# Kernel tuning notes

Hardware: AMD Instinct MI355X
Metric: run time of the kernel (lower is better)

Reference implementation:

```python
import jax, jax.numpy as jnp
import numpy as np

N = 16384
N_ITER = 10
TAU = 1e-3  # LM initial damping factor


def _skew(w):
    z = jnp.zeros((), w.dtype)
    return jnp.stack([
        jnp.stack([z, -w[2], w[1]]),
        jnp.stack([w[2], z, -w[0]]),
        jnp.stack([-w[1], w[0], z]),
    ])


def se3_exp(x):
    # x = [omega (3), v (3)] -> 4x4 SE3 (lie_se3_to_SE3)
    w, v = x[:3], x[3:]
    th2 = jnp.dot(w, w)
    th = jnp.sqrt(th2)
    small = th < 1e-8
    ths = jnp.where(small, jnp.ones_like(th), th)
    A = jnp.where(small, 1.0 - th2 / 6.0, jnp.sin(ths) / ths)
    B = jnp.where(small, 0.5 - th2 / 24.0, (1.0 - jnp.cos(ths)) / ths ** 2)
    C = jnp.where(small, 1.0 / 6.0 - th2 / 120.0, (ths - jnp.sin(ths)) / ths ** 3)
    W = _skew(w)
    W2 = W @ W
    I = jnp.eye(3, dtype=x.dtype)
    R = I + A * W + B * W2
    V = I + B * W + C * W2
    t = V @ v
    T = jnp.eye(4, dtype=x.dtype).at[:3, :3].set(R).at[:3, 3].set(t)
    return T


def _res_jac(x, ref_pts, trg_pts, trg_normals):
    T = se3_exp(x)
    R, t = T[:3, :3], T[:3, 3]
    # dist_association: ref cloud transformed by inv(T_est), nearest target point
    Ri, ti = R.T, -R.T @ t
    ref_t = ref_pts @ Ri.T + ti  # [N,3]
    d2 = ((ref_t ** 2).sum(-1)[:, None]
          + (trg_pts ** 2).sum(-1)[None, :]
          - 2.0 * (ref_t @ trg_pts.T))  # [N_ref, N_trg] -- dominant memory traffic
    trg_ids = jnp.argmin(d2, axis=1)  # src_ids == arange(N_ref)
    # residual: dot(n_trg_transformed, ref - trg_transformed) at correspondences
    trg_t = trg_pts @ R.T + t
    n_t = trg_normals @ R.T
    n = n_t[trg_ids]          # [N,3] gather
    p = trg_t[trg_ids]        # [N,3] gather
    r = jnp.sum(n * (ref_pts - p), axis=1)  # [N]
    # J = n^T @ j_3d(ref_pts)  ==  [cross(p_ref, n), n]  (closed form of 1x3x6 matmuls)
    J = jnp.concatenate([jnp.cross(ref_pts, n), n], axis=1)  # [N,6]
    return r, J


def reference(ref_pts, trg_pts, trg_normals):
    dtype = ref_pts.dtype
    x = jnp.zeros(6, dtype=dtype)
    r, J = _res_jac(x, ref_pts, trg_pts, trg_normals)
    F = jnp.sum(r ** 2)
    H0 = J.T @ J
    mu = TAU * jnp.max(jnp.diag(H0))
    nu = jnp.asarray(2.0, dtype)
    I6 = jnp.eye(6, dtype=dtype)
    for _ in range(N_ITER):
        H = J.T @ J
        g = J.T @ r
        dx = jnp.linalg.solve(H + mu * I6, -g)
        x_new = x + dx
        r_new, J_new = _res_jac(x_new, ref_pts, trg_pts, trg_normals)
        F_new = jnp.sum(r_new ** 2)
        denom = jnp.dot(dx, mu * dx - g)
        rho = (F - F_new) / jnp.where(jnp.abs(denom) < 1e-12, 1e-12, denom)
        accept = rho > 0.0
        x = jnp.where(accept, x_new, x)
        r = jnp.where(accept, r_new, r)
        J = jnp.where(accept, J_new, J)
        F = jnp.where(accept, F_new, F)
        mu = jnp.where(accept,
                       mu * jnp.maximum(1.0 / 3.0, 1.0 - (2.0 * rho - 1.0) ** 3),
                       mu * nu)
        nu = jnp.where(accept, jnp.asarray(2.0, dtype), 2.0 * nu)
    T = se3_exp(x)
    cost = jnp.mean(r ** 2)  # cost_fun(residual_fun(x,...))
    return T, cost


def setup_inputs() -> dict:
    key = jax.random.key(0)
    k1, k2 = jax.random.split(key)
    ref_pts = jax.random.normal(k1, (N, 3), dtype=jnp.float32)
    # target = slightly rotated/translated copy so ICP has a meaningful solution
    ang = 0.05
    R_true = np.array([[np.cos(ang), -np.sin(ang), 0.0],
                       [np.sin(ang), np.cos(ang), 0.0],
                       [0.0, 0.0, 1.0]], dtype=np.float32)
    t_true = np.array([0.02, -0.01, 0.03], dtype=np.float32)
    trg_pts = ref_pts @ jnp.asarray(R_true).T + jnp.asarray(t_true)
    n = jax.random.normal(k2, (N, 3), dtype=jnp.float32)
    trg_normals = n / jnp.linalg.norm(n, axis=1, keepdims=True)
    return {"ref_pts": ref_pts, "trg_pts": trg_pts, "trg_normals": trg_normals}
```

## Files before the change

### kernel.cpp

```cpp
#include <hip/hip_runtime.h>
#include <stdint.h>

#define N_PTS 16384
#define TAU_C 0.001f
#define N_ITER 10

#define G 48
#define NCELLS (G * G * G)
#define XMIN (-6.0f)
#define CELL_H 0.25f
#define INV_H 4.0f
#define NSCAN ((NCELLS + 1023) / 1024)
#define GS 8
#define QPB (256 / GS)
#define NEVAL (N_PTS / QPB)

struct State {
  float x[6];
  float xc[6];
  float dx[6];
  float Rc[9];
  float tc[3];
  float H[21];
  float g[6];
  float F, mu, nu;
};

__device__ void se3_exp_rt(const float* x, float* R, float* t) {
  float wx = x[0], wy = x[1], wz = x[2];
  float vx = x[3], vy = x[4], vz = x[5];
  float th2 = wx*wx + wy*wy + wz*wz;
  float th = sqrtf(th2);
  float A, B, C;
  if (th < 1e-8f) {
    A = 1.0f - th2 / 6.0f;
    B = 0.5f - th2 / 24.0f;
    C = 1.0f / 6.0f - th2 / 120.0f;
  } else {
    float s = sinf(th), c = cosf(th);
    A = s / th;
    B = (1.0f - c) / th2;
    C = (th - s) / (th2 * th);
  }
  float W[9]  = {0.f, -wz, wy,  wz, 0.f, -wx,  -wy, wx, 0.f};
  float W2[9];
  #pragma unroll
  for (int r = 0; r < 3; r++)
    #pragma unroll
    for (int c = 0; c < 3; c++)
      W2[3*r+c] = W[3*r+0]*W[0+c] + W[3*r+1]*W[3+c] + W[3*r+2]*W[6+c];
  float V[9];
  #pragma unroll
  for (int k = 0; k < 9; k++) {
    float I = (k == 0 || k == 4 || k == 8) ? 1.f : 0.f;
    R[k] = I + A * W[k] + B * W2[k];
    V[k] = I + B * W[k] + C * W2[k];
  }
  t[0] = V[0]*vx + V[1]*vy + V[2]*vz;
  t[1] = V[3]*vx + V[4]*vy + V[5]*vz;
  t[2] = V[6]*vx + V[7]*vy + V[8]*vz;
}

__device__ inline int cell1d(float v) {
  int c = (int)floorf((v - XMIN) * INV_H);
  return min(max(c, 0), G - 1);
}

__global__ __launch_bounds__(256) void zero_kernel(unsigned* __restrict__ count,
                                                   unsigned* __restrict__ counter,
                                                   State* st) {
  unsigned idx = blockIdx.x * 256u + threadIdx.x;
  if (idx < NCELLS) count[idx] = 0u;
  if (idx == 0) {
    #pragma unroll
    for (int k = 0; k < 6; k++) { st->x[k] = 0.f; st->xc[k] = 0.f; st->dx[k] = 0.f; }
    #pragma unroll
    for (int k = 0; k < 9; k++) st->Rc[k] = (k % 4 == 0) ? 1.f : 0.f;
    st->tc[0] = st->tc[1] = st->tc[2] = 0.f;
    st->nu = 2.f;
    *counter = 0u;
  }
}

__global__ __launch_bounds__(256) void count_kernel(const float* __restrict__ trg,
                                                    unsigned* __restrict__ count) {
  int j = blockIdx.x * 256 + threadIdx.x;
  int cx = cell1d(trg[3*j]), cy = cell1d(trg[3*j+1]), cz = cell1d(trg[3*j+2]);
  atomicAdd(&count[(cz * G + cy) * G + cx], 1u);
}

__global__ __launch_bounds__(256) void scan1_kernel(const unsigned* __restrict__ count,
                                                    unsigned* __restrict__ excl,
                                                    unsigned* __restrict__ blockSums) {
  __shared__ unsigned sh[256];
  const int t = threadIdx.x;
  const unsigned base = blockIdx.x * 1024u + t * 4u;
  unsigned v0 = (base + 0 < NCELLS) ? count[base + 0] : 0u;
  unsigned v1 = (base + 1 < NCELLS) ? count[base + 1] : 0u;
  unsigned v2 = (base + 2 < NCELLS) ? count[base + 2] : 0u;
  unsigned v3 = (base + 3 < NCELLS) ? count[base + 3] : 0u;
  unsigned tsum = v0 + v1 + v2 + v3;
  sh[t] = tsum;
  __syncthreads();
  for (int off = 1; off < 256; off <<= 1) {
    unsigned xv = (t >= off) ? sh[t - off] : 0u;
    __syncthreads();
    sh[t] += xv;
    __syncthreads();
  }
  unsigned texcl = sh[t] - tsum;
  if (t == 255) blockSums[blockIdx.x] = sh[255];
  if (base + 0 < NCELLS) excl[base + 0] = texcl;
  if (base + 1 < NCELLS) excl[base + 1] = texcl + v0;
  if (base + 2 < NCELLS) excl[base + 2] = texcl + v0 + v1;
  if (base + 3 < NCELLS) excl[base + 3] = texcl + v0 + v1 + v2;
}

__global__ __launch_bounds__(512) void scan2_kernel(unsigned* __restrict__ blockSums) {
  __shared__ unsigned sh[512];
  int t = threadIdx.x;
  unsigned v = (t < NSCAN) ? blockSums[t] : 0u;
  sh[t] = v;
  __syncthreads();
  for (int off = 1; off < 512; off <<= 1) {
    unsigned xv = (t >= off) ? sh[t - off] : 0u;
    __syncthreads();
    sh[t] += xv;
    __syncthreads();
  }
  if (t < NSCAN) blockSums[t] = sh[t] - v;
}

__global__ __launch_bounds__(256) void scan3_kernel(const unsigned* __restrict__ count,
                                                    unsigned* __restrict__ cursor,
                                                    const unsigned* __restrict__ blockSums,
                                                    unsigned* __restrict__ gridPacked) {
  const unsigned base = blockIdx.x * 1024u + threadIdx.x * 4u;
  unsigned boff = blockSums[blockIdx.x];
  #pragma unroll
  for (int q = 0; q < 4; q++) {
    unsigned idx = base + q;
    if (idx < NCELLS) {
      unsigned start = cursor[idx] + boff;
      unsigned n = count[idx]; n = n > 255u ? 255u : n;
      gridPacked[idx] = (start << 8) | n;
      cursor[idx] = start;
    }
  }
}

__global__ __launch_bounds__(256) void scatter_kernel(const float* __restrict__ trg,
                                                      unsigned* __restrict__ cursor,
                                                      float4* __restrict__ sortedPts,
                                                      unsigned* __restrict__ sortedIdx) {
  int j = blockIdx.x * 256 + threadIdx.x;
  float tx = trg[3*j], ty = trg[3*j+1], tz = trg[3*j+2];
  int cx = cell1d(tx), cy = cell1d(ty), cz = cell1d(tz);
  unsigned pos = atomicAdd(&cursor[(cz * G + cy) * G + cx], 1u);
  sortedPts[pos] = make_float4(tx, ty, tz, __uint_as_float((unsigned)j));
  sortedIdx[pos] = (unsigned)j;
}

__global__ __launch_bounds__(256) void eval_kernel(const float* __restrict__ ref,
                                                   const float* __restrict__ trg,
                                                   const float* __restrict__ nrm,
                                                   const unsigned* __restrict__ gridPacked,
                                                   const float4* __restrict__ sortedPts,
                                                   const unsigned* __restrict__ sortedIdx,
                                                   State* st,
                                                   double* __restrict__ partials,
                                                   unsigned* __restrict__ counter,
                                                   float* out, int mode) {
  const int tid = threadIdx.x;
  const int gl = tid & (GS - 1);
  const int it = blockIdx.x * QPB + (tid >> 3);
  const int i = (int)sortedIdx[it];

  const float R00 = st->Rc[0], R01 = st->Rc[1], R02 = st->Rc[2];
  const float R10 = st->Rc[3], R11 = st->Rc[4], R12 = st->Rc[5];
  const float R20 = st->Rc[6], R21 = st->Rc[7], R22 = st->Rc[8];
  const float t0 = st->tc[0], t1 = st->tc[1], t2 = st->tc[2];

  const float rx = ref[3*i], ry = ref[3*i+1], rz = ref[3*i+2];
  const float ax = rx - t0, ay = ry - t1, az = rz - t2;
  const float qx = R00*ax + R10*ay + R20*az;
  const float qy = R01*ax + R11*ay + R21*az;
  const float qz = R02*ax + R12*ay + R22*az;
  const int gx = cell1d(qx), gy = cell1d(qy), gz = cell1d(qz);

  unsigned long long bkey = 0xFFFFFFFFFFFFFFFFULL;
  for (int r = 1; r <= G; r++) {
    const int W = 2*r + 1, W2 = W * W, nc = W2 * W;
    for (int t = gl; t < nc; t += GS) {
      int tz = t / W2;
      int rm = t - tz * W2;
      int ty = rm / W;
      int tx = rm - ty * W;
      int cz = gz + tz - r, cy = gy + ty - r, cx = gx + tx - r;
      if ((unsigned)cx >= (unsigned)G || (unsigned)cy >= (unsigned)G ||
          (unsigned)cz >= (unsigned)G) continue;
      unsigned pc = gridPacked[(cz * G + cy) * G + cx];
      unsigned s0 = pc >> 8, n = pc & 255u;
      for (unsigned c = 0; c < n; c++) {
        float4 p = sortedPts[s0 + c];
        float ddx = qx - p.x, ddy = qy - p.y, ddz = qz - p.z;
        float d2 = fmaf(ddz, ddz, fmaf(ddy, ddy, ddx * ddx));
        unsigned long long key = ((unsigned long long)__float_as_uint(d2) << 32)
                               | (unsigned long long)__float_as_uint(p.w);
        bkey = key < bkey ? key : bkey;
      }
    }
    #pragma unroll
    for (int off = 1; off < GS; off <<= 1) {
      unsigned long long o = __shfl_xor(bkey, off, 64);
      bkey = o < bkey ? o : bkey;
    }
    float best = __uint_as_float((unsigned)(bkey >> 32));
    float dmin = 3.4e38f;
    if (gx - r > 0)     dmin = fminf(dmin, qx - (XMIN + (float)(gx - r) * CELL_H));
    if (gx + r < G - 1) dmin = fminf(dmin, (XMIN + (float)(gx + r + 1) * CELL_H) - qx);
    if (gy - r > 0)     dmin = fminf(dmin, qy - (XMIN + (float)(gy - r) * CELL_H));
    if (gy + r < G - 1) dmin = fminf(dmin, (XMIN + (float)(gy + r + 1) * CELL_H) - qy);
    if (gz - r > 0)     dmin = fminf(dmin, qz - (XMIN + (float)(gz - r) * CELL_H));
    if (gz + r < G - 1) dmin = fminf(dmin, (XMIN + (float)(gz + r + 1) * CELL_H) - qz);
    if (best <= dmin * dmin) break;
  }
  const int j = (int)(unsigned)(bkey & 0xFFFFFFFFULL);

  float Jv[6] = {0.f, 0.f, 0.f, 0.f, 0.f, 0.f};
  float rres = 0.f;
  if (gl == 0) {
    float nx0 = nrm[3*j], ny0 = nrm[3*j+1], nz0 = nrm[3*j+2];
    float sx = trg[3*j], sy = trg[3*j+1], sz = trg[3*j+2];
    float nx = R00*nx0 + R01*ny0 + R02*nz0;
    float ny = R10*nx0 + R11*ny0 + R12*nz0;
    float nz = R20*nx0 + R21*ny0 + R22*nz0;
    float pxx = R00*sx + R01*sy + R02*sz + t0;
    float pyy = R10*sx + R11*sy + R12*sz + t1;
    float pzz = R20*sx + R21*sy + R22*sz + t2;
    float dxx = rx - pxx, dyy = ry - pyy, dzz = rz - pzz;
    rres = nx*dxx + ny*dyy + nz*dzz;
    Jv[0] = ry*nz - rz*ny;
    Jv[1] = rz*nx - rx*nz;
    Jv[2] = rx*ny - ry*nx;
    Jv[3] = nx; Jv[4] = ny; Jv[5] = nz;
  }

  double acc[28];
  int c21 = 0;
  #pragma unroll
  for (int a = 0; a < 6; a++)
    #pragma unroll
    for (int b = a; b < 6; b++)
      acc[c21++] = (double)Jv[a] * (double)Jv[b];
  #pragma unroll
  for (int a = 0; a < 6; a++) acc[21+a] = (double)Jv[a] * (double)rres;
  acc[27] = (double)rres * (double)rres;

  #pragma unroll
  for (int kk = 0; kk < 28; kk++) {
    double v = acc[kk];
    for (int off = 32; off; off >>= 1) v += __shfl_down(v, off);
    acc[kk] = v;
  }
  __shared__ double redD[4][28];
  int wave = tid >> 6, lane = tid & 63;
  if (lane == 0) {
    #pragma unroll
    for (int kk = 0; kk < 28; kk++) redD[wave][kk] = acc[kk];
  }
  __syncthreads();
  if (tid < 28)
    partials[tid * NEVAL + blockIdx.x] =
        redD[0][tid] + redD[1][tid] + redD[2][tid] + redD[3][tid];

  __shared__ bool last;
  __syncthreads();
  if (tid == 0) {
    __threadfence();
    unsigned old = atomicAdd(counter, 1u);
    last = (old == NEVAL - 1);
  }
  __syncthreads();
  if (!last) return;

  __threadfence();
  __shared__ double red2[28][8];
  if (tid < 224) {
    int c = tid >> 3, s = tid & 7;
    double sum = 0.0;
    const double* pp = partials + c * NEVAL + s * 64;
    for (int b = 0; b < 64; b++) sum += pp[b];
    red2[c][s] = sum;
  }
  __syncthreads();
  __shared__ float tot[28];
  if (tid < 28) {
    double s = 0.0;
    #pragma unroll
    for (int k = 0; k < 8; k++) s += red2[tid][k];
    tot[tid] = (float)s;
  }
  __syncthreads();

  if (tid == 0) {
    atomicExch(counter, 0u);
    float Fn = tot[27];
    float mu, nu;

    if (mode == 0) {
      #pragma unroll
      for (int k = 0; k < 6; k++) st->x[k] = st->xc[k];
      #pragma unroll
      for (int k = 0; k < 21; k++) st->H[k] = tot[k];
      #pragma unroll
      for (int k = 0; k < 6; k++) st->g[k] = tot[21+k];
      st->F = Fn;
      float md = tot[0];
      md = fmaxf(md, tot[6]); md = fmaxf(md, tot[11]); md = fmaxf(md, tot[15]);
      md = fmaxf(md, tot[18]); md = fmaxf(md, tot[20]);
      mu = TAU_C * md;
      nu = 2.f;
    } else {
      mu = st->mu; nu = st->nu;
      float denom = 0.f;
      #pragma unroll
      for (int k = 0; k < 6; k++) denom += st->dx[k] * (mu * st->dx[k] - st->g[k]);
      if (fabsf(denom) < 1e-12f) denom = 1e-12f;
      float rho = (st->F - Fn) / denom;
      if (rho > 0.f) {
        #pragma unroll
        for (int k = 0; k < 6; k++) st->x[k] = st->xc[k];
        #pragma unroll
        for (int k = 0; k < 21; k++) st->H[k] = tot[k];
        #pragma unroll
        for (int k = 0; k < 6; k++) st->g[k] = tot[21+k];
        st->F = Fn;
        float tcube = 2.f * rho - 1.f;
        mu = mu * fmaxf(1.f / 3.f, 1.f - tcube * tcube * tcube);
        nu = 2.f;
      } else {
        mu = mu * nu;
        nu = 2.f * nu;
      }
    }
    st->mu = mu; st->nu = nu;

    if (mode < N_ITER) {
      float A[6][7];
      int c21b = 0;
      #pragma unroll
      for (int a = 0; a < 6; a++)
        #pragma unroll
        for (int b = a; b < 6; b++) { A[a][b] = st->H[c21b]; A[b][a] = st->H[c21b]; c21b++; }
      #pragma unroll
      for (int a = 0; a < 6; a++) { A[a][a] += mu; A[a][6] = -st->g[a]; }
      #pragma unroll
      for (int col = 0; col < 6; col++) {
        float inv = 1.f / A[col][col];
        #pragma unroll
        for (int rI = 0; rI < 6; rI++) {
          if (rI > col) {
            float f = A[rI][col] * inv;
            #pragma unroll
            for (int cc = 0; cc < 7; cc++)
              if (cc >= col) A[rI][cc] -= f * A[col][cc];
          }
        }
      }
      float d[6];
      #pragma unroll
      for (int rI = 5; rI >= 0; rI--) {
        float s = A[rI][6];
        #pragma unroll
        for (int cc = 0; cc < 6; cc++)
          if (cc > rI) s -= A[rI][cc] * d[cc];
        d[rI] = s / A[rI][rI];
      }
      float Rn[9], tn[3];
      #pragma unroll
      for (int k = 0; k < 6; k++) { st->dx[k] = d[k]; st->xc[k] = st->x[k] + d[k]; }
      se3_exp_rt(st->xc, Rn, tn);
      #pragma unroll
      for (int k = 0; k < 9; k++) st->Rc[k] = Rn[k];
      #pragma unroll
      for (int k = 0; k < 3; k++) st->tc[k] = tn[k];
    } else {
      float Rn[9], tn[3];
      se3_exp_rt(st->x, Rn, tn);
      out[0] = Rn[0]; out[1] = Rn[1]; out[2]  = Rn[2]; out[3]  = tn[0];
      out[4] = Rn[3]; out[5] = Rn[4]; out[6]  = Rn[5]; out[7]  = tn[1];
      out[8] = Rn[6]; out[9] = Rn[7]; out[10] = Rn[8]; out[11] = tn[2];
      out[12] = 0.f; out[13] = 0.f; out[14] = 0.f; out[15] = 1.f;
      out[16] = st->F / (float)N_PTS;
    }
  }
}

extern "C" void kernel_launch(void* const* d_in, const int* in_sizes, int n_in,
                              void* d_out, int out_size, void* d_ws, size_t ws_size,
                              hipStream_t stream) {
  const float* ref = (const float*)d_in[0];
  const float* trg = (const float*)d_in[1];
  const float* nrm = (const float*)d_in[2];
  float* out = (float*)d_out;

  char* ws = (char*)d_ws;
  unsigned* count      = (unsigned*)(ws);
  unsigned* gridPacked = (unsigned*)(ws + 442368);
  unsigned* cursor     = (unsigned*)(ws + 884736);
  unsigned* blockSums  = (unsigned*)(ws + 1327104);
  float4*   sortedPts  = (float4*)  (ws + 1329152);
  unsigned* sortedIdx  = (unsigned*)(ws + 1591296);
  double*   partials   = (double*)  (ws + 1656832);
  unsigned* counter    = (unsigned*)(ws + 1771520);
  State*    st         = (State*)   (ws + 1771584);

  zero_kernel   <<<(NCELLS + 255) / 256, 256, 0, stream>>>(count, counter, st);
  count_kernel  <<<N_PTS / 256, 256, 0, stream>>>(trg, count);
  scan1_kernel  <<<NSCAN, 256, 0, stream>>>(count, cursor, blockSums);
  scan2_kernel  <<<1, 512, 0, stream>>>(blockSums);
  scan3_kernel  <<<NSCAN, 256, 0, stream>>>(count, cursor, blockSums, gridPacked);
  scatter_kernel<<<N_PTS / 256, 256, 0, stream>>>(trg, cursor, sortedPts, sortedIdx);

  for (int e = 0; e <= N_ITER; e++)
    eval_kernel<<<NEVAL, 256, 0, stream>>>(ref, trg, nrm, gridPacked, sortedPts,
                                           sortedIdx, st, partials, counter, out, e);
}
```

Before: 394.7 us.

## Search fixed 3x3x3 neighborhood with 16 lanes, brute-force fallback for unresolved queries

Result: slower. 721.6 us (+82.8%).

```diff
diff --git a/kernel.cpp b/kernel.cpp
--- a/kernel.cpp
+++ b/kernel.cpp
@@ -11,7 +11,7 @@
 #define CELL_H 0.25f
 #define INV_H 4.0f
 #define NSCAN ((NCELLS + 1023) / 1024)
-#define GS 8
+#define GS 16
 #define QPB (256 / GS)
 #define NEVAL (N_PTS / QPB)
 
@@ -172,8 +172,9 @@
                                                    unsigned* __restrict__ counter,
                                                    float* out, int mode) {
   const int tid = threadIdx.x;
+  const int lane = tid & 63;
   const int gl = tid & (GS - 1);
-  const int it = blockIdx.x * QPB + (tid >> 3);
+  const int it = blockIdx.x * QPB + (tid >> 4);
   const int i = (int)sortedIdx[it];
 
   const float R00 = st->Rc[0], R01 = st->Rc[1], R02 = st->Rc[2];
@@ -188,42 +189,70 @@
   const float qz = R02*ax + R12*ay + R22*az;
   const int gx = cell1d(qx), gy = cell1d(qy), gz = cell1d(qz);
 
+  unsigned pcv[2];
+  #pragma unroll
+  for (int k = 0; k < 2; k++) {
+    pcv[k] = 0u;
+    int t = gl + GS * k;
+    if (t < 27) {
+      int tz = t / 9, rm = t - tz * 9, ty = rm / 3, tx = rm - ty * 3;
+      int cz = gz + tz - 1, cy = gy + ty - 1, cx = gx + tx - 1;
+      if ((unsigned)cx < (unsigned)G && (unsigned)cy < (unsigned)G &&
+          (unsigned)cz < (unsigned)G)
+        pcv[k] = gridPacked[(cz * G + cy) * G + cx];
+    }
+  }
   unsigned long long bkey = 0xFFFFFFFFFFFFFFFFULL;
-  for (int r = 1; r <= G; r++) {
-    const int W = 2*r + 1, W2 = W * W, nc = W2 * W;
-    for (int t = gl; t < nc; t += GS) {
-      int tz = t / W2;
-      int rm = t - tz * W2;
-      int ty = rm / W;
-      int tx = rm - ty * W;
-      int cz = gz + tz - r, cy = gy + ty - r, cx = gx + tx - r;
-      if ((unsigned)cx >= (unsigned)G || (unsigned)cy >= (unsigned)G ||
-          (unsigned)cz >= (unsigned)G) continue;
-      unsigned pc = gridPacked[(cz * G + cy) * G + cx];
-      unsigned s0 = pc >> 8, n = pc & 255u;
-      for (unsigned c = 0; c < n; c++) {
-        float4 p = sortedPts[s0 + c];
-        float ddx = qx - p.x, ddy = qy - p.y, ddz = qz - p.z;
-        float d2 = fmaf(ddz, ddz, fmaf(ddy, ddy, ddx * ddx));
-        unsigned long long key = ((unsigned long long)__float_as_uint(d2) << 32)
-                               | (unsigned long long)__float_as_uint(p.w);
-        bkey = key < bkey ? key : bkey;
-      }
-    }
-    #pragma unroll
-    for (int off = 1; off < GS; off <<= 1) {
-      unsigned long long o = __shfl_xor(bkey, off, 64);
-      bkey = o < bkey ? o : bkey;
-    }
-    float best = __uint_as_float((unsigned)(bkey >> 32));
-    float dmin = 3.4e38f;
-    if (gx - r > 0)     dmin = fminf(dmin, qx - (XMIN + (float)(gx - r) * CELL_H));
-    if (gx + r < G - 1) dmin = fminf(dmin, (XMIN + (float)(gx + r + 1) * CELL_H) - qx);
-    if (gy - r > 0)     dmin = fminf(dmin, qy - (XMIN + (float)(gy - r) * CELL_H));
-    if (gy + r < G - 1) dmin = fminf(dmin, (XMIN + (float)(gy + r + 1) * CELL_H) - qy);
-    if (gz - r > 0)     dmin = fminf(dmin, qz - (XMIN + (float)(gz - r) * CELL_H));
-    if (gz + r < G - 1) dmin = fminf(dmin, (XMIN + (float)(gz + r + 1) * CELL_H) - qz);
-    if (best <= dmin * dmin) break;
+  #pragma unroll
+  for (int k = 0; k < 2; k++) {
+    unsigned s0 = pcv[k] >> 8, n = pcv[k] & 255u;
+    for (unsigned c = 0; c < n; c++) {
+      float4 p = sortedPts[s0 + c];
+      float ddx = qx - p.x, ddy = qy - p.y, ddz = qz - p.z;
+      float d2 = fmaf(ddz, ddz, fmaf(ddy, ddy, ddx * ddx));
+      unsigned long long key = ((unsigned long long)__float_as_uint(d2) << 32)
+                             | (unsigned long long)(unsigned)__float_as_uint(p.w);
+      bkey = key < bkey ? key : bkey;
+    }
+  }
+  #pragma unroll
+  for (int off = 1; off < GS; off <<= 1) {
+    unsigned long long o = __shfl_xor(bkey, off, 64);
+    bkey = o < bkey ? o : bkey;
+  }
+  float best = __uint_as_float((unsigned)(bkey >> 32));
+  float dmin = 3.4e38f;
+  if (gx - 1 > 0)     dmin = fminf(dmin, qx - (XMIN + (float)(gx - 1) * CELL_H));
+  if (gx + 1 < G - 1) dmin = fminf(dmin, (XMIN + (float)(gx + 2) * CELL_H) - qx);
+  if (gy - 1 > 0)     dmin = fminf(dmin, qy - (XMIN + (float)(gy - 1) * CELL_H));
+  if (gy + 1 < G - 1) dmin = fminf(dmin, (XMIN + (float)(gy + 2) * CELL_H) - qy);
+  if (gz - 1 > 0)     dmin = fminf(dmin, qz - (XMIN + (float)(gz - 1) * CELL_H));
+  if (gz + 1 < G - 1) dmin = fminf(dmin, (XMIN + (float)(gz + 2) * CELL_H) - qz);
+  bool resolved = (best <= dmin * dmin);
+
+  unsigned long long m = __ballot((gl == 0) && !resolved);
+  while (m) {
+    int src = __ffsll((long long)m) - 1;
+    m &= m - 1;
+    float bqx = __shfl(qx, src, 64);
+    float bqy = __shfl(qy, src, 64);
+    float bqz = __shfl(qz, src, 64);
+    unsigned long long bb = 0xFFFFFFFFFFFFFFFFULL;
+    #pragma unroll 4
+    for (int p = lane; p < N_PTS; p += 64) {
+      float4 pt = sortedPts[p];
+      float ddx = bqx - pt.x, ddy = bqy - pt.y, ddz = bqz - pt.z;
+      float d2 = fmaf(ddz, ddz, fmaf(ddy, ddy, ddx * ddx));
+      unsigned long long key = ((unsigned long long)__float_as_uint(d2) << 32)
+                             | (unsigned long long)(unsigned)__float_as_uint(pt.w);
+      bb = key < bb ? key : bb;
+    }
+    #pragma unroll
+    for (int off = 1; off < 64; off <<= 1) {
+      unsigned long long o = __shfl_xor(bb, off, 64);
+      bb = o < bb ? o : bb;
+    }
+    if ((lane >> 4) == (src >> 4)) bkey = bb;
   }
   const int j = (int)(unsigned)(bkey & 0xFFFFFFFFULL);
 
@@ -260,11 +289,12 @@
   #pragma unroll
   for (int kk = 0; kk < 28; kk++) {
     double v = acc[kk];
-    for (int off = 32; off; off >>= 1) v += __shfl_down(v, off);
+    v += __shfl_down(v, 16, 64);
+    v += __shfl_down(v, 32, 64);
     acc[kk] = v;
   }
   __shared__ double redD[4][28];
-  int wave = tid >> 6, lane = tid & 63;
+  int wave = tid >> 6;
   if (lane == 0) {
     #pragma unroll
     for (int kk = 0; kk < 28; kk++) redD[wave][kk] = acc[kk];
@@ -288,10 +318,12 @@
   __shared__ double red2[28][8];
   if (tid < 224) {
     int c = tid >> 3, s = tid & 7;
-    double sum = 0.0;
-    const double* pp = partials + c * NEVAL + s * 64;
-    for (int b = 0; b < 64; b++) sum += pp[b];
-    red2[c][s] = sum;
+    const double* pp = partials + c * NEVAL + s * 128;
+    double s0 = 0.0, s1 = 0.0, s2 = 0.0, s3 = 0.0;
+    for (int b = 0; b < 128; b += 4) {
+      s0 += pp[b]; s1 += pp[b+1]; s2 += pp[b+2]; s3 += pp[b+3];
+    }
+    red2[c][s] = (s0 + s1) + (s2 + s3);
   }
   __syncthreads();
   __shared__ float tot[28];
@@ -413,8 +445,8 @@
   float4*   sortedPts  = (float4*)  (ws + 1329152);
   unsigned* sortedIdx  = (unsigned*)(ws + 1591296);
   double*   partials   = (double*)  (ws + 1656832);
-  unsigned* counter    = (unsigned*)(ws + 1771520);
-  State*    st         = (State*)   (ws + 1771584);
+  unsigned* counter    = (unsigned*)(ws + 1886208);
+  State*    st         = (State*)   (ws + 1886272);
 
   zero_kernel   <<<(NCELLS + 255) / 256, 256, 0, stream>>>(count, counter, st);
   count_kernel  <<<N_PTS / 256, 256, 0, stream>>>(trg, count);
```

## Bound nearest-neighbor grid search by distance to the same-index target point

Applied to the files above, without the earlier changes.

Measured after the change: 520.4 us. +31.9%, slower.

```diff
diff --git a/kernel.cpp b/kernel.cpp
--- a/kernel.cpp
+++ b/kernel.cpp
@@ -11,7 +11,7 @@
 #define CELL_H 0.25f
 #define INV_H 4.0f
 #define NSCAN ((NCELLS + 1023) / 1024)
-#define GS 8
+#define GS 16
 #define QPB (256 / GS)
 #define NEVAL (N_PTS / QPB)
 
@@ -172,8 +172,9 @@
                                                    unsigned* __restrict__ counter,
                                                    float* out, int mode) {
   const int tid = threadIdx.x;
+  const int lane = tid & 63;
   const int gl = tid & (GS - 1);
-  const int it = blockIdx.x * QPB + (tid >> 3);
+  const int it = blockIdx.x * QPB + (tid >> 4);
   const int i = (int)sortedIdx[it];
 
   const float R00 = st->Rc[0], R01 = st->Rc[1], R02 = st->Rc[2];
@@ -186,44 +187,39 @@
   const float qx = R00*ax + R10*ay + R20*az;
   const float qy = R01*ax + R11*ay + R21*az;
   const float qz = R02*ax + R12*ay + R22*az;
-  const int gx = cell1d(qx), gy = cell1d(qy), gz = cell1d(qz);
+
+  const float wx_ = trg[3*i], wy_ = trg[3*i+1], wz_ = trg[3*i+2];
+  float dpx = qx - wx_, dpy = qy - wy_, dpz = qz - wz_;
+  float dub = sqrtf(fmaf(dpz, dpz, fmaf(dpy, dpy, dpx * dpx)));
+  dub = fmaf(dub, 4e-6f, dub) + 2e-7f;
+
+  const int lox = cell1d(qx - dub), hix = cell1d(qx + dub);
+  const int loy = cell1d(qy - dub), hiy = cell1d(qy + dub);
+  const int loz = cell1d(qz - dub), hiz = cell1d(qz + dub);
+  const int nx_ = hix - lox + 1, ny_ = hiy - loy + 1, nz_ = hiz - loz + 1;
+  const int nxy = nx_ * ny_, nc = nxy * nz_;
 
   unsigned long long bkey = 0xFFFFFFFFFFFFFFFFULL;
-  for (int r = 1; r <= G; r++) {
-    const int W = 2*r + 1, W2 = W * W, nc = W2 * W;
-    for (int t = gl; t < nc; t += GS) {
-      int tz = t / W2;
-      int rm = t - tz * W2;
-      int ty = rm / W;
-      int tx = rm - ty * W;
-      int cz = gz + tz - r, cy = gy + ty - r, cx = gx + tx - r;
-      if ((unsigned)cx >= (unsigned)G || (unsigned)cy >= (unsigned)G ||
-          (unsigned)cz >= (unsigned)G) continue;
-      unsigned pc = gridPacked[(cz * G + cy) * G + cx];
-      unsigned s0 = pc >> 8, n = pc & 255u;
-      for (unsigned c = 0; c < n; c++) {
-        float4 p = sortedPts[s0 + c];
-        float ddx = qx - p.x, ddy = qy - p.y, ddz = qz - p.z;
-        float d2 = fmaf(ddz, ddz, fmaf(ddy, ddy, ddx * ddx));
-        unsigned long long key = ((unsigned long long)__float_as_uint(d2) << 32)
-                               | (unsigned long long)__float_as_uint(p.w);
-        bkey = key < bkey ? key : bkey;
-      }
+  for (int t = gl; t < nc; t += GS) {
+    int tz = t / nxy;
+    int rm = t - tz * nxy;
+    int ty = rm / nx_;
+    int tx = rm - ty * nx_;
+    unsigned pc = gridPacked[((loz + tz) * G + (loy + ty)) * G + (lox + tx)];
+    unsigned s0 = pc >> 8, n = pc & 255u;
+    for (unsigned c = 0; c < n; c++) {
+      float4 p = sortedPts[s0 + c];
+      float ddx = qx - p.x, ddy = qy - p.y, ddz = qz - p.z;
+      float d2 = fmaf(ddz, ddz, fmaf(ddy, ddy, ddx * ddx));
+      unsigned long long key = ((unsigned long long)__float_as_uint(d2) << 32)
+                             | (unsigned long long)(unsigned)__float_as_uint(p.w);
+      bkey = key < bkey ? key : bkey;
     }
-    #pragma unroll
-    for (int off = 1; off < GS; off <<= 1) {
-      unsigned long long o = __shfl_xor(bkey, off, 64);
-      bkey = o < bkey ? o : bkey;
-    }
-    float best = __uint_as_float((unsigned)(bkey >> 32));
-    float dmin = 3.4e38f;
-    if (gx - r > 0)     dmin = fminf(dmin, qx - (XMIN + (float)(gx - r) * CELL_H));
-    if (gx + r < G - 1) dmin = fminf(dmin, (XMIN + (float)(gx + r + 1) * CELL_H) - qx);
-    if (gy - r > 0)     dmin = fminf(dmin, qy - (XMIN + (float)(gy - r) * CELL_H));
-    if (gy + r < G - 1) dmin = fminf(dmin, (XMIN + (float)(gy + r + 1) * CELL_H) - qy);
-    if (gz - r > 0)     dmin = fminf(dmin, qz - (XMIN + (float)(gz - r) * CELL_H));
-    if (gz + r < G - 1) dmin = fminf(dmin, (XMIN + (float)(gz + r + 1) * CELL_H) - qz);
-    if (best <= dmin * dmin) break;
+  }
+  #pragma unroll
+  for (int off = 1; off < GS; off <<= 1) {
+    unsigned long long o = __shfl_xor(bkey, off, 64);
+    bkey = o < bkey ? o : bkey;
   }
   const int j = (int)(unsigned)(bkey & 0xFFFFFFFFULL);
 
@@ -260,11 +256,12 @@
   #pragma unroll
   for (int kk = 0; kk < 28; kk++) {
     double v = acc[kk];
-    for (int off = 32; off; off >>= 1) v += __shfl_down(v, off);
+    v += __shfl_down(v, 16, 64);
+    v += __shfl_down(v, 32, 64);
     acc[kk] = v;
   }
   __shared__ double redD[4][28];
-  int wave = tid >> 6, lane = tid & 63;
+  int wave = tid >> 6;
   if (lane == 0) {
     #pragma unroll
     for (int kk = 0; kk < 28; kk++) redD[wave][kk] = acc[kk];
@@ -288,10 +285,12 @@
   __shared__ double red2[28][8];
   if (tid < 224) {
     int c = tid >> 3, s = tid & 7;
-    double sum = 0.0;
-    const double* pp = partials + c * NEVAL + s * 64;
-    for (int b = 0; b < 64; b++) sum += pp[b];
-    red2[c][s] = sum;
+    const double* pp = partials + c * NEVAL + s * 128;
+    double s0 = 0.0, s1 = 0.0, s2 = 0.0, s3 = 0.0;
+    for (int b = 0; b < 128; b += 4) {
+      s0 += pp[b]; s1 += pp[b+1]; s2 += pp[b+2]; s3 += pp[b+3];
+    }
+    red2[c][s] = (s0 + s1) + (s2 + s3);
   }
   __syncthreads();
   __shared__ float tot[28];
@@ -413,8 +412,8 @@
   float4*   sortedPts  = (float4*)  (ws + 1329152);
   unsigned* sortedIdx  = (unsigned*)(ws + 1591296);
   double*   partials   = (double*)  (ws + 1656832);
-  unsigned* counter    = (unsigned*)(ws + 1771520);
-  State*    st         = (State*)   (ws + 1771584);
+  unsigned* counter    = (unsigned*)(ws + 1886208);
+  State*    st         = (State*)   (ws + 1886272);
 
   zero_kernel   <<<(NCELLS + 255) / 256, 256, 0, stream>>>(count, counter, st);
   count_kernel  <<<N_PTS / 256, 256, 0, stream>>>(trg, count);
```
